# Performance work log

Measured on AMD Instinct MI355X. Metric: run time of the kernel, lower is better.

Reference implementation:

```python
import jax, jax.numpy as jnp
import numpy as np

BITS_W = 2  # WAGE default weight bitwidth


def _scale(bits):
    return 2.0 ** (bits - 1)


def quantize_w(x):
    """WAGE Quantize.W: clip to [-1+delta, 1-delta], round to grid of step delta,
    with straight-through estimator for gradients."""
    s = _scale(BITS_W)
    delta = 1.0 / s
    xc = jnp.clip(x, -1.0 + delta, 1.0 - delta)
    y = jnp.round(xc * s) / s
    # straight-through: forward uses y, gradient flows as identity to x
    return x + jax.lax.stop_gradient(y - x)


def setup_inputs() -> dict:
    key = jax.random.key(0)
    k1, k2 = jax.random.split(key)
    B, D_IN, C_OUT = 16384, 1024, 1024
    inputs = jax.random.normal(k1, (B, D_IN), dtype=jnp.float32)
    # learned kernel per build(): shape [d_in, c_out]
    kernel = jax.random.normal(k2, (D_IN, C_OUT), dtype=jnp.float32) * 0.5
    return {"inputs": inputs, "kernel": kernel}


def reference(inputs, kernel):
    # quantize weights every forward pass, then dense matmul
    return jnp.matmul(inputs, quantize_w(kernel))
```

## Files before the change

kernel.cpp:

```cpp
#include <hip/hip_runtime.h>

typedef unsigned short u16;
typedef unsigned int u32;

typedef __bf16 bf16x8 __attribute__((ext_vector_type(8)));
typedef float floatx4 __attribute__((ext_vector_type(4)));


__device__ __forceinline__ u32 f2bf(float f) {
    u32 u = __builtin_bit_cast(u32, f);
    return (u + 0x7fffu + ((u >> 16) & 1u)) >> 16;
}

__device__ __forceinline__ float quant_w(float x) {
    float xc = fminf(fmaxf(x, -0.5f), 0.5f);
    return rintf(xc * 2.0f) * 0.5f;
}

__device__ __forceinline__ void gload_lds16(const u16* g, u16* l) {
    __builtin_amdgcn_global_load_lds(
        (const __attribute__((address_space(1))) void*)g,
        (__attribute__((address_space(3))) void*)l,
        16, 0, 0);
}


__global__ __launch_bounds__(256) void cast_a_kernel(const float4* __restrict__ in,
                                                     uint4* __restrict__ out) {
    int t = blockIdx.x * 256 + threadIdx.x;
#pragma unroll
    for (int u = 0; u < 2; u++) {
        float4 a = in[4 * t + 2 * u];
        float4 b = in[4 * t + 2 * u + 1];
        uint4 o;
        o.x = f2bf(a.x) | (f2bf(a.y) << 16);
        o.y = f2bf(a.z) | (f2bf(a.w) << 16);
        o.z = f2bf(b.x) | (f2bf(b.y) << 16);
        o.w = f2bf(b.z) | (f2bf(b.w) << 16);
        out[2 * t + u] = o;
    }
}


__global__ __launch_bounds__(256) void quant_transpose_kernel(const float* __restrict__ W,
                                                              u16* __restrict__ Bt) {
    __shared__ u16 tile[32][33];
    const int KN = 1024;
    int tx = threadIdx.x;
    int ty = threadIdx.y;
    int k0 = blockIdx.y * 32;
    int n0 = blockIdx.x * 32;
#pragma unroll
    for (int i = 0; i < 4; i++) {
        int kl = ty + i * 8;
        float x = W[(k0 + kl) * KN + n0 + tx];
        tile[kl][tx] = (u16)f2bf(quant_w(x));
    }
    __syncthreads();
#pragma unroll
    for (int i = 0; i < 4; i++) {
        int nl = ty + i * 8;
        Bt[(n0 + nl) * KN + k0 + tx] = tile[tx][nl];
    }
}


__global__ __launch_bounds__(512, 2) void gemm_2region_kernel(const u16* __restrict__ A,
                                                              const u16* __restrict__ Bt,
                                                              float* __restrict__ C) {
    const int K = 1024;
    const int N = 1024;

    __shared__ alignas(16) u16 As[2 * 2 * 128 * 64];
    __shared__ alignas(16) u16 Bs[2 * 2 * 128 * 64];

    const int tid = threadIdx.x;
    const int lane = tid & 63;
    const int wid = tid >> 6;
    const int wm = wid >> 2;
    const int wn = wid & 3;
    const int frow = lane & 15;
    const int fkc = lane >> 4;
    const int rsw = frow & 7;
    const int mbase = blockIdx.x * 256;
    const int nbase = blockIdx.y * 256;

    const int sr = tid >> 3;
    const int gc = (tid & 7) ^ (sr & 7);
    const int brow0 = ((sr >> 5) << 6) | (sr & 31);

    floatx4 acc[8][4] = {};
    bf16x8 af0[4][2], af1[4][2], bf0[2][2], bf1[2][2];

    auto astage = [&](int tau, int u) {
        const int row = sr + u * 64;
#pragma unroll
        for (int hf = 0; hf < 2; hf++) {
            const u16* g = &A[(size_t)(mbase + hf * 128 + row) * K + (size_t)tau * 64 + gc * 8];
            u16* dst = &As[(((tau & 1) * 2 + hf) * 8192) + row * 64 + (tid & 7) * 8];
            gload_lds16(g, dst);
        }
    };
    auto bstage = [&](int tau, int u) {
        const int row = brow0 + u * 32;
#pragma unroll
        for (int hf = 0; hf < 2; hf++) {
            const u16* g = &Bt[(size_t)(nbase + hf * 128 + row) * K + (size_t)tau * 64 + gc * 8];
            u16* dst = &Bs[(((tau & 1) * 2 + hf) * 8192) + row * 64 + (tid & 7) * 8];
            gload_lds16(g, dst);
        }
    };

#define LGKM0() asm volatile("s_waitcnt lgkmcnt(0)" ::: "memory")
#define VMC(n)  asm volatile("s_waitcnt vmcnt(" #n ")" ::: "memory")
#define BAR()                          \
    __builtin_amdgcn_sched_barrier(0); \
    __builtin_amdgcn_s_barrier();      \
    __builtin_amdgcn_sched_barrier(0)

#define READ_AF0(b)                                                                  \
    _Pragma("unroll") for (int mf = 0; mf < 4; mf++)                                 \
        _Pragma("unroll") for (int s = 0; s < 2; s++)                                \
            af0[mf][s] = *(const bf16x8*)&As[(((b)*2 + wm) * 128 + mf * 16 + frow) * 64 + \
                                             (((s * 4 + fkc) ^ rsw) * 8)]
#define READ_AF1(b)                                                                  \
    _Pragma("unroll") for (int mf = 0; mf < 4; mf++)                                 \
        _Pragma("unroll") for (int s = 0; s < 2; s++)                                \
            af1[mf][s] = *(const bf16x8*)&As[(((b)*2 + wm) * 128 + 64 + mf * 16 + frow) * 64 + \
                                             (((s * 4 + fkc) ^ rsw) * 8)]
#define READ_BF0(b)                                                                  \
    _Pragma("unroll") for (int nf = 0; nf < 2; nf++)                                 \
        _Pragma("unroll") for (int s = 0; s < 2; s++)                                \
            bf0[nf][s] = *(const bf16x8*)&Bs[(((b)*2 + (wn >> 1)) * 128 + (wn & 1) * 64 + nf * 16 + frow) * 64 + \
                                             (((s * 4 + fkc) ^ rsw) * 8)]
#define READ_BF1(b)                                                                  \
    _Pragma("unroll") for (int nf = 0; nf < 2; nf++)                                 \
        _Pragma("unroll") for (int s = 0; s < 2; s++)                                \
            bf1[nf][s] = *(const bf16x8*)&Bs[(((b)*2 + (wn >> 1)) * 128 + (wn & 1) * 64 + 32 + nf * 16 + frow) * 64 + \
                                             (((s * 4 + fkc) ^ rsw) * 8)]
#define MFMA_CL(af, bf, mo, no)                                                      \
    __builtin_amdgcn_s_setprio(1);                                                   \
    _Pragma("unroll") for (int mf = 0; mf < 4; mf++)                                 \
        _Pragma("unroll") for (int nf = 0; nf < 2; nf++)                             \
            _Pragma("unroll") for (int s = 0; s < 2; s++)                            \
                acc[(mo) + mf][(no) + nf] = __builtin_amdgcn_mfma_f32_16x16x32_bf16( \
                    af[mf][s], bf[nf][s], acc[(mo) + mf][(no) + nf], 0, 0, 0);       \
    __builtin_amdgcn_s_setprio(0)

    astage(0, 0); bstage(0, 0);
    astage(0, 1); bstage(0, 1);
    astage(1, 0); bstage(1, 0);
    VMC(8);
    BAR();

    for (int t = 0; t < 16; t++) {
        const int b = t & 1;

        if (t > 0) { MFMA_CL(af1, bf1, 4, 2); }
        READ_AF0(b);
        READ_BF0(b);
        if (t <= 14) {
            astage(t + 1, 1); bstage(t + 1, 1);
            VMC(8);
        } else {
            VMC(0);
        }
        LGKM0();
        BAR();

        READ_AF1(b);
        READ_BF1(b);
        MFMA_CL(af0, bf0, 0, 0);
        MFMA_CL(af1, bf0, 4, 0);
        MFMA_CL(af0, bf1, 0, 2);
        if (t <= 13) {
            astage(t + 2, 0); bstage(t + 2, 0);
            VMC(8);
        } else if (t == 14) {
            VMC(4);
        }
        LGKM0();
        BAR();
    }

    MFMA_CL(af1, bf1, 4, 2);

#undef LGKM0
#undef VMC
#undef BAR
#undef READ_AF0
#undef READ_AF1
#undef READ_BF0
#undef READ_BF1
#undef MFMA_CL

    const int crow = (lane >> 4) * 4;
    const int ccol = lane & 15;
#pragma unroll
    for (int i = 0; i < 8; i++) {
#pragma unroll
        for (int j = 0; j < 4; j++) {
            float* cp = &C[(size_t)(mbase + wm * 128 + i * 16 + crow) * N +
                           nbase + wn * 64 + j * 16 + ccol];
#pragma unroll
            for (int r = 0; r < 4; r++) cp[r * N] = acc[i][j][r];
        }
    }
}


extern "C" void kernel_launch(void* const* d_in, const int* in_sizes, int n_in,
                              void* d_out, int out_size, void* d_ws, size_t ws_size,
                              hipStream_t stream) {
    const float* A = (const float*)d_in[0];
    const float* W = (const float*)d_in[1];
    float* C = (float*)d_out;

    u16* Abf = (u16*)d_ws;
    u16* Btq = (u16*)((char*)d_ws + (size_t)33554432);

    cast_a_kernel<<<4096, 256, 0, stream>>>((const float4*)A, (uint4*)Abf);
    quant_transpose_kernel<<<dim3(32, 32), dim3(32, 8), 0, stream>>>(W, Btq);
    gemm_2region_kernel<<<dim3(64, 4), 512, 0, stream>>>(Abf, Btq, C);
}
```

Baseline: 147.2 us.

## Restructure GEMM main loop into eight barrier-separated phases interleaving loads and MFMA

Splits each K-step of the bf16 MFMA GEMM into four read/MFMA phases, each ending in a barrier. Every phase issues one quarter of the global-to-LDS prefetch and then one MFMA cluster. The aim is to spread memory traffic more evenly between compute bursts and keep the workgroup's waves in lockstep, instead of the previous two-phase schedule. The cost is roughly four times as many barriers per iteration. Dropping the sched_barrier fences also lets the compiler move instructions across them, which risks wrong vmcnt accounting or extra stalls.

```diff
diff --git a/kernel.cpp b/kernel.cpp
--- a/kernel.cpp
+++ b/kernel.cpp
@@ -65,9 +65,9 @@
 }
 
 
-__global__ __launch_bounds__(512, 2) void gemm_2region_kernel(const u16* __restrict__ A,
-                                                              const u16* __restrict__ Bt,
-                                                              float* __restrict__ C) {
+__global__ __launch_bounds__(512, 2) void gemm_8phase_v2_kernel(const u16* __restrict__ A,
+                                                                const u16* __restrict__ Bt,
+                                                                float* __restrict__ C) {
     const int K = 1024;
     const int N = 1024;
 
@@ -93,30 +93,27 @@
     bf16x8 af0[4][2], af1[4][2], bf0[2][2], bf1[2][2];
 
     auto astage = [&](int tau, int u) {
-        const int row = sr + u * 64;
+        const int r = u * 64 + sr;
 #pragma unroll
         for (int hf = 0; hf < 2; hf++) {
-            const u16* g = &A[(size_t)(mbase + hf * 128 + row) * K + (size_t)tau * 64 + gc * 8];
-            u16* dst = &As[(((tau & 1) * 2 + hf) * 8192) + row * 64 + (tid & 7) * 8];
+            const u16* g = &A[(size_t)(mbase + hf * 128 + r) * K + (size_t)tau * 64 + gc * 8];
+            u16* dst = &As[(((tau & 1) * 2 + hf) * 8192) + r * 64 + (tid & 7) * 8];
             gload_lds16(g, dst);
         }
     };
     auto bstage = [&](int tau, int u) {
-        const int row = brow0 + u * 32;
+        const int r = brow0 + u * 32;
 #pragma unroll
         for (int hf = 0; hf < 2; hf++) {
-            const u16* g = &Bt[(size_t)(nbase + hf * 128 + row) * K + (size_t)tau * 64 + gc * 8];
-            u16* dst = &Bs[(((tau & 1) * 2 + hf) * 8192) + row * 64 + (tid & 7) * 8];
+            const u16* g = &Bt[(size_t)(nbase + hf * 128 + r) * K + (size_t)tau * 64 + gc * 8];
+            u16* dst = &Bs[(((tau & 1) * 2 + hf) * 8192) + r * 64 + (tid & 7) * 8];
             gload_lds16(g, dst);
         }
     };
 
-#define LGKM0() asm volatile("s_waitcnt lgkmcnt(0)" ::: "memory")
-#define VMC(n)  asm volatile("s_waitcnt vmcnt(" #n ")" ::: "memory")
-#define BAR()                          \
-    __builtin_amdgcn_sched_barrier(0); \
-    __builtin_amdgcn_s_barrier();      \
-    __builtin_amdgcn_sched_barrier(0)
+#define CLOB_LGKM() asm volatile("s_waitcnt lgkmcnt(0)" ::: "memory")
+#define CLOB_VM(n)  asm volatile("s_waitcnt vmcnt(" #n ")" ::: "memory")
+#define SB()        __builtin_amdgcn_s_barrier()
 
 #define READ_AF0(b)                                                                  \
     _Pragma("unroll") for (int mf = 0; mf < 4; mf++)                                 \
@@ -147,47 +144,50 @@
                     af[mf][s], bf[nf][s], acc[(mo) + mf][(no) + nf], 0, 0, 0);       \
     __builtin_amdgcn_s_setprio(0)
 
-    astage(0, 0); bstage(0, 0);
-    astage(0, 1); bstage(0, 1);
+    astage(0, 0); bstage(0, 0); bstage(0, 1); astage(0, 1);
     astage(1, 0); bstage(1, 0);
-    VMC(8);
-    BAR();
+    CLOB_VM(4);
+    SB();
 
     for (int t = 0; t < 16; t++) {
         const int b = t & 1;
 
-        if (t > 0) { MFMA_CL(af1, bf1, 4, 2); }
         READ_AF0(b);
         READ_BF0(b);
-        if (t <= 14) {
-            astage(t + 1, 1); bstage(t + 1, 1);
-            VMC(8);
-        } else {
-            VMC(0);
-        }
-        LGKM0();
-        BAR();
+        if (t <= 14) bstage(t + 1, 1);
+        CLOB_LGKM();
+        SB();
+        MFMA_CL(af0, bf0, 0, 0);
+        SB();
+
+        READ_BF1(b);
+        if (t <= 14) astage(t + 1, 1);
+        CLOB_LGKM();
+        SB();
+        MFMA_CL(af0, bf1, 0, 2);
+        SB();
 
         READ_AF1(b);
-        READ_BF1(b);
-        MFMA_CL(af0, bf0, 0, 0);
+        if (t <= 13) astage(t + 2, 0);
+        CLOB_LGKM();
+        SB();
         MFMA_CL(af1, bf0, 4, 0);
-        MFMA_CL(af0, bf1, 0, 2);
+        SB();
+
         if (t <= 13) {
-            astage(t + 2, 0); bstage(t + 2, 0);
-            VMC(8);
+            bstage(t + 2, 0);
+            CLOB_VM(4);
         } else if (t == 14) {
-            VMC(4);
-        }
-        LGKM0();
-        BAR();
-    }
-
-    MFMA_CL(af1, bf1, 4, 2);
-
-#undef LGKM0
-#undef VMC
-#undef BAR
+            CLOB_VM(0);
+        }
+        SB();
+        MFMA_CL(af1, bf1, 4, 2);
+        SB();
+    }
+
+#undef CLOB_LGKM
+#undef CLOB_VM
+#undef SB
 #undef READ_AF0
 #undef READ_AF1
 #undef READ_BF0
@@ -221,5 +221,5 @@
 
     cast_a_kernel<<<4096, 256, 0, stream>>>((const float4*)A, (uint4*)Abf);
     quant_transpose_kernel<<<dim3(32, 32), dim3(32, 8), 0, stream>>>(W, Btq);
-    gemm_2region_kernel<<<dim3(64, 4), 512, 0, stream>>>(Abf, Btq, C);
-}
+    gemm_8phase_v2_kernel<<<dim3(64, 4), 512, 0, stream>>>(Abf, Btq, C);
+}
```

Measured after the change: 147.6 us. About the same (+0.3%).
